# Optimization experiments

Measured on AMD Instinct MI355X. Metric: run time of the kernel, lower is better.

The kernel has to match this reference:

```python
import jax, jax.numpy as jnp
import numpy as np

B, N, D, H, L = 2, 2048, 512, 8, 2
HD = D // H


def setup_inputs() -> dict:
    key = jax.random.key(0)
    ks = jax.random.split(key, 8)
    s = 0.02
    return {
        "inputs_embeds": jax.random.normal(ks[0], (B, N, D), jnp.float32),
        "pos_emb": jax.random.normal(ks[1], (N, D), jnp.float32) * s,
        "c_attn_w": jax.random.normal(ks[2], (L, D, 3 * D), jnp.float32) * s,
        "c_attn_b": jnp.zeros((L, 3 * D), jnp.float32),
        "out_w": jax.random.normal(ks[3], (L, D, D), jnp.float32) * s,
        "out_b": jnp.zeros((L, D), jnp.float32),
        "ln1_g": jnp.ones((L, D), jnp.float32),
        "ln1_b": jnp.zeros((L, D), jnp.float32),
        "c_fc_w": jax.random.normal(ks[4], (L, D, 4 * D), jnp.float32) * s,
        "c_fc_b": jnp.zeros((L, 4 * D), jnp.float32),
        "c_proj_w": jax.random.normal(ks[5], (L, 4 * D, D), jnp.float32) * s,
        "c_proj_b": jnp.zeros((L, D), jnp.float32),
        "ln2_g": jnp.ones((L, D), jnp.float32),
        "ln2_b": jnp.zeros((L, D), jnp.float32),
    }


def _layernorm(x, g, b, eps=1e-5):
    mu = jnp.mean(x, axis=-1, keepdims=True)
    var = jnp.mean(jnp.square(x - mu), axis=-1, keepdims=True)
    return (x - mu) * jax.lax.rsqrt(var + eps) * g + b


def _gelu_new(x):
    # NewGELUActivation: tanh approximation
    return 0.5 * x * (1.0 + jnp.tanh(jnp.sqrt(2.0 / jnp.pi) * (x + 0.044715 * x ** 3)))


def _attention(x, w_qkv, b_qkv, w_out, b_out, self_mask):
    qkv = x @ w_qkv + b_qkv                      # [B,N,3D]
    q, k, v = jnp.split(qkv, 3, axis=-1)
    def heads(t):
        return t.reshape(B, N, H, HD).transpose(0, 2, 1, 3)  # [B,H,N,HD]
    q, k, v = heads(q), heads(k), heads(v)
    scores = jnp.einsum('bhqd,bhkd->bhqk', q, k) / jnp.sqrt(jnp.float32(HD))
    neg = jnp.finfo(scores.dtype).min
    scores = jnp.where(self_mask, scores, neg)   # exclude-self mask
    attn = jax.nn.softmax(scores, axis=-1)
    o = jnp.einsum('bhqk,bhkd->bhqd', attn, v)
    o = o.transpose(0, 2, 1, 3).reshape(B, N, D)
    return o @ w_out + b_out


def reference(inputs_embeds, pos_emb, c_attn_w, c_attn_b, out_w, out_b,
              ln1_g, ln1_b, c_fc_w, c_fc_b, c_proj_w, c_proj_b, ln2_g, ln2_b):
    self_mask = ~jnp.eye(N, dtype=bool)[None, None]  # [1,1,N,N]
    h = inputs_embeds + pos_emb[None]
    for l in range(L):
        res = h
        x = _layernorm(h, ln1_g[l], ln1_b[l])
        h = _attention(x, c_attn_w[l], c_attn_b[l], out_w[l], out_b[l], self_mask) + res
        res = h
        x = _layernorm(h, ln2_g[l], ln2_b[l])
        x = _gelu_new(x @ c_fc_w[l] + c_fc_b[l])
        h = (x @ c_proj_w[l] + c_proj_b[l]) + res
    return h
```

## Files before the change

kernel.cpp:

```cpp
#include <hip/hip_runtime.h>
#include <hip/hip_bf16.h>
#include <math.h>

#define BB 2
#define NN 2048
#define DD 512
#define HH 8
#define LL 2
#define TT (BB*NN)

typedef short short8 __attribute__((ext_vector_type(8)));
typedef float floatx4 __attribute__((ext_vector_type(4)));

__device__ __forceinline__ unsigned short f2b(float v) {
    union { float f; unsigned u; } x; x.f = v;
    unsigned r = x.u + 0x7fff + ((x.u >> 16) & 1);
    return (unsigned short)(r >> 16);
}

__device__ __forceinline__ void gld16(const unsigned short* g, unsigned short* lds) {
    __builtin_amdgcn_global_load_lds(
        (const __attribute__((address_space(1))) unsigned int*)g,
        (__attribute__((address_space(3))) unsigned int*)lds,
        16, 0, 0);
}

__global__ __launch_bounds__(256) void k_bias_add(const float* __restrict__ src,
                                                  const float* __restrict__ bias,
                                                  float* __restrict__ dst) {
    int i = blockIdx.x * 256 + threadIdx.x;
    dst[i] = src[i] + bias[i & (DD - 1)];
}

template <int EMB>
__global__ __launch_bounds__(256) void k_ln(const float* __restrict__ hin,
                                            unsigned short* __restrict__ xout,
                                            const float* __restrict__ g,
                                            const float* __restrict__ b,
                                            const float* __restrict__ emb,
                                            const float* __restrict__ pos,
                                            float* __restrict__ hout) {
    __shared__ float red[4];
    __shared__ float bc1, bc2;
    int t = blockIdx.x;
    int tid = threadIdx.x;
    int lane = tid & 63, wv = tid >> 6;
    float v0, v1;
    if (EMB) {
        const float* erow = emb + (size_t)t * DD;
        const float* prow = pos + (size_t)(t & (NN - 1)) * DD;
        v0 = erow[tid] + prow[tid];
        v1 = erow[tid + 256] + prow[tid + 256];
        hout[(size_t)t * DD + tid] = v0;
        hout[(size_t)t * DD + tid + 256] = v1;
    } else {
        const float* row = hin + (size_t)t * DD;
        v0 = row[tid];
        v1 = row[tid + 256];
    }

    float s = v0 + v1;
#pragma unroll
    for (int o = 32; o; o >>= 1) s += __shfl_down(s, o, 64);
    if (lane == 0) red[wv] = s;
    __syncthreads();
    if (tid == 0) bc1 = (red[0] + red[1] + red[2] + red[3]) * (1.0f / DD);
    __syncthreads();
    float mu = bc1;
    float d0 = v0 - mu, d1 = v1 - mu;
    s = d0 * d0 + d1 * d1;
#pragma unroll
    for (int o = 32; o; o >>= 1) s += __shfl_down(s, o, 64);
    if (lane == 0) red[wv] = s;
    __syncthreads();
    if (tid == 0) bc2 = (red[0] + red[1] + red[2] + red[3]) * (1.0f / DD);
    __syncthreads();
    float rstd = rsqrtf(bc2 + 1e-5f);
    xout[(size_t)t * DD + tid]       = f2b(d0 * rstd * g[tid] + b[tid]);
    xout[(size_t)t * DD + tid + 256] = f2b(d1 * rstd * g[tid + 256] + b[tid + 256]);
}

__device__ __forceinline__ float gelu_new(float v) {
    const float c = 0.7978845608028654f;
    float u = c * (v + 0.044715f * v * v * v);
    u = fminf(fmaxf(u, -30.0f), 30.0f);
    float e = __builtin_amdgcn_exp2f(2.885390081777927f * u);
    return v * e * __builtin_amdgcn_rcpf(e + 1.0f);
}

#define PL 3145728
__global__ __launch_bounds__(256) void k_wt_all(const float* __restrict__ c_attn_w,
                                                const float* __restrict__ out_w,
                                                const float* __restrict__ c_fc_w,
                                                const float* __restrict__ c_proj_w,
                                                unsigned short* __restrict__ wbuf) {
    __shared__ unsigned short t[64][72];
    int bx = blockIdx.x;
    int l = bx / 768;
    int r = bx - l * 768;
    const float* W; unsigned short* WT; int K, N;
    if (r < 192)      { W = c_attn_w + (size_t)l * 512 * 1536; WT = wbuf + (size_t)l * PL;           K = 512;  N = 1536; }
    else if (r < 256) { r -= 192; W = out_w  + (size_t)l * 512 * 512;  WT = wbuf + (size_t)l * PL + 786432;  K = 512;  N = 512; }
    else if (r < 512) { r -= 256; W = c_fc_w + (size_t)l * 512 * 2048; WT = wbuf + (size_t)l * PL + 1048576; K = 512;  N = 2048; }
    else              { r -= 512; W = c_proj_w + (size_t)l * 2048 * 512; WT = wbuf + (size_t)l * PL + 2097152; K = 2048; N = 512; }
    int tiles_n = N >> 6;
    int n0 = (r % tiles_n) * 64, k0 = (r / tiles_n) * 64;

    int tid = threadIdx.x;
    int rr = tid >> 2;
    int c0 = (tid & 3) * 16;
    const float* src = W + (size_t)(k0 + rr) * N + n0 + c0;
#pragma unroll
    for (int u = 0; u < 4; u++) {
        float4 v = *(const float4*)&src[u * 4];
        t[c0 + u * 4 + 0][rr] = f2b(v.x);
        t[c0 + u * 4 + 1][rr] = f2b(v.y);
        t[c0 + u * 4 + 2][rr] = f2b(v.z);
        t[c0 + u * 4 + 3][rr] = f2b(v.w);
    }
    __syncthreads();
    unsigned short* dst = WT + (size_t)(n0 + rr) * K + k0 + c0;
#pragma unroll
    for (int u = 0; u < 4; u++)
        *(uint2*)&dst[u * 4] = *(const uint2*)&t[rr][c0 + u * 4];
}

template <int ACT, int BF16OUT, int ATOMIC>
__global__ __launch_bounds__(512) void k_mgemm(const unsigned short* __restrict__ Ab,
                                               const unsigned short* __restrict__ Bt,
                                               const float* __restrict__ bias,
                                               float* __restrict__ Cp,
                                               unsigned short* __restrict__ Cb,
                                               int Kfull, int Kchunk, int N) {
    __shared__ unsigned short Als[2][16 * 512];
    __shared__ unsigned short Bls[2][16 * 512];

    int tid = threadIdx.x;
    int l = tid & 63, w = tid >> 6;
    int wm = w >> 2, wn = w & 3;
    int m0 = blockIdx.y * 128, n0 = blockIdx.x * 128;
    int kb = blockIdx.z * Kchunk;
    int lr = l & 15;
    int lk = (l >> 4) * 8;

    const unsigned short* Ap = Ab + (size_t)(m0 + w * 16 + lr) * Kfull + kb + lk;
    const unsigned short* Bp = Bt + (size_t)(n0 + w * 16 + lr) * Kfull + kb + lk;
    unsigned short* lsA = &Als[0][0];
    unsigned short* lsB = &Bls[0][0];
    int wbase = w << 9;
    const int KH = 8 * 512;
    const int BUF = 16 * 512;

    floatx4 acc[4][2];
#pragma unroll
    for (int i = 0; i < 4; i++)
#pragma unroll
        for (int j = 0; j < 2; j++) acc[i][j] = (floatx4){0.f, 0.f, 0.f, 0.f};

    int nit = Kchunk >> 6;

    gld16(Ap,      lsA + wbase);
    gld16(Ap + 32, lsA + KH + wbase);
    gld16(Bp,      lsB + wbase);
    gld16(Bp + 32, lsB + KH + wbase);
    __syncthreads();

    for (int it = 0; it < nit; it++) {
        int c = it & 1;
        if (it + 1 < nit) {
            int ko = (it + 1) << 6;
            int db = (c ^ 1) * BUF;
            gld16(Ap + ko,      lsA + db + wbase);
            gld16(Ap + ko + 32, lsA + db + KH + wbase);
            gld16(Bp + ko,      lsB + db + wbase);
            gld16(Bp + ko + 32, lsB + db + KH + wbase);
        }
        int cb = c * BUF;
#pragma unroll
        for (int kk = 0; kk < 2; kk++) {
            short8 a[4], b[2];
            int ko = cb + kk * KH;
#pragma unroll
            for (int i = 0; i < 4; i++)
                a[i] = *(const short8*)&lsA[ko + (wm * 4 + i) * 512 + l * 8];
#pragma unroll
            for (int j = 0; j < 2; j++)
                b[j] = *(const short8*)&lsB[ko + (wn * 2 + j) * 512 + l * 8];
#pragma unroll
            for (int i = 0; i < 4; i++)
#pragma unroll
                for (int j = 0; j < 2; j++)
                    acc[i][j] = __builtin_amdgcn_mfma_f32_16x16x32_bf16(a[i], b[j], acc[i][j], 0, 0, 0);
        }
        __syncthreads();
    }

    int col_in = l & 15, rquad = (l >> 4) * 4;
    bool addb = (!ATOMIC) || (bias != nullptr && blockIdx.z == 0);
#pragma unroll
    for (int i = 0; i < 4; i++) {
        int gm_base = m0 + wm * 64 + i * 16 + rquad;
#pragma unroll
        for (int j = 0; j < 2; j++) {
            int gn = n0 + wn * 32 + j * 16 + col_in;
            float bv = addb ? bias[gn] : 0.0f;
#pragma unroll
            for (int r = 0; r < 4; r++) {
                size_t off = (size_t)(gm_base + r) * N + gn;
                if (ATOMIC) {
                    atomicAdd(&Cp[off], acc[i][j][r] + bv);
                } else {
                    float v = acc[i][j][r] + bv;
                    if (ACT) v = gelu_new(v);
                    if (BF16OUT) Cb[off] = f2b(v);
                    else Cp[off] = v;
                }
            }
        }
    }
}

__global__ __launch_bounds__(256) void k_attn_mfma(const unsigned short* __restrict__ qkv,
                                                   unsigned short* __restrict__ xatt) {
    __shared__ unsigned short Ks[2][64 * 72];
    __shared__ unsigned short Vt[2][64 * 72];
    __shared__ unsigned short Pls[64 * 72];

    int qt = blockIdx.x, hd = blockIdx.y, b = blockIdx.z;
    int tid = threadIdx.x;
    int l = tid & 63, w = tid >> 6;
    int lr = l & 15, quad = l >> 4;

    const size_t base = (size_t)b * NN * 1536;

    short8 qf[2];
    {
        const unsigned short* qrow = qkv + base + (size_t)(qt * 64 + w * 16 + lr) * 1536 + hd * 64;
        qf[0] = *(const short8*)&qrow[quad * 8];
        qf[1] = *(const short8*)&qrow[quad * 8 + 32];
    }

    floatx4 O[4];
#pragma unroll
    for (int jd = 0; jd < 4; jd++) O[jd] = (floatx4){0.f, 0.f, 0.f, 0.f};
    float lsum = 0.0f;

    int sr = tid >> 2, sc = (tid & 3) * 16;
    int vk = (tid & 15) * 4, vd = (tid >> 4) * 4;
    const int STEP = 64 * 1536;
    const unsigned short* Kp = qkv + base + 512 + hd * 64 + (size_t)sr * 1536 + sc;
    const unsigned short* Vp = qkv + base + 1024 + hd * 64 + (size_t)vk * 1536 + vd;

    uint4 rk0, rk1;
    union { uint2 u; unsigned short s[4]; } rv[4];

    rk0 = *(const uint4*)Kp;
    rk1 = *(const uint4*)(Kp + 8);
#pragma unroll
    for (int i = 0; i < 4; i++)
        rv[i].u = *(const uint2*)(Vp + (size_t)i * 1536);
    *(uint4*)&Ks[0][sr * 72 + sc]     = rk0;
    *(uint4*)&Ks[0][sr * 72 + sc + 8] = rk1;
#pragma unroll
    for (int j = 0; j < 4; j++) {
        union { uint2 u; unsigned short s[4]; } pk;
        pk.s[0] = rv[0].s[j]; pk.s[1] = rv[1].s[j];
        pk.s[2] = rv[2].s[j]; pk.s[3] = rv[3].s[j];
        *(uint2*)&Vt[0][(vd + j) * 72 + vk] = pk.u;
    }
    Kp += STEP; Vp += STEP;
    rk0 = *(const uint4*)Kp;
    rk1 = *(const uint4*)(Kp + 8);
#pragma unroll
    for (int i = 0; i < 4; i++)
        rv[i].u = *(const uint2*)(Vp + (size_t)i * 1536);
    __syncthreads();

    const float EC1 = 0.18033688011112042f;
    const float EC0 = -11.541560327111707f;

    for (int kt = 0; kt < 32; kt++) {
        int c = kt & 1;

        floatx4 s[4];
#pragma unroll
        for (int jn = 0; jn < 4; jn++) s[jn] = (floatx4){0.f, 0.f, 0.f, 0.f};
#pragma unroll
        for (int ss = 0; ss < 2; ss++)
#pragma unroll
            for (int jn = 0; jn < 4; jn++) {
                short8 ak = *(const short8*)&Ks[c][(jn * 16 + lr) * 72 + ss * 32 + quad * 8];
                s[jn] = __builtin_amdgcn_mfma_f32_16x16x32_bf16(ak, qf[ss], s[jn], 0, 0, 0);
            }

        int mq = w * 16 + lr;
        bool diag = (kt == qt);
#pragma unroll
        for (int jn = 0; jn < 4; jn++) {
            float p0 = __builtin_amdgcn_exp2f(fmaf(s[jn][0], EC1, EC0));
            float p1 = __builtin_amdgcn_exp2f(fmaf(s[jn][1], EC1, EC0));
            float p2 = __builtin_amdgcn_exp2f(fmaf(s[jn][2], EC1, EC0));
            float p3 = __builtin_amdgcn_exp2f(fmaf(s[jn][3], EC1, EC0));
            if (diag) {
                int kbase = jn * 16 + quad * 4;
                if (mq == kbase + 0) p0 = 0.0f;
                if (mq == kbase + 1) p1 = 0.0f;
                if (mq == kbase + 2) p2 = 0.0f;
                if (mq == kbase + 3) p3 = 0.0f;
            }
            lsum += (p0 + p1) + (p2 + p3);
            unsigned w01, w23;
            asm("v_cvt_pk_bf16_f32 %0, %1, %2" : "=v"(w01) : "v"(p0), "v"(p1));
            asm("v_cvt_pk_bf16_f32 %0, %1, %2" : "=v"(w23) : "v"(p2), "v"(p3));
            uint2 pku; pku.x = w01; pku.y = w23;
            *(uint2*)&Pls[mq * 72 + jn * 16 + quad * 4] = pku;
        }

#pragma unroll
        for (int ss = 0; ss < 2; ss++) {
            short8 ap = *(const short8*)&Pls[(w * 16 + lr) * 72 + ss * 32 + quad * 8];
#pragma unroll
            for (int jd = 0; jd < 4; jd++) {
                short8 bv = *(const short8*)&Vt[c][(jd * 16 + lr) * 72 + ss * 32 + quad * 8];
                O[jd] = __builtin_amdgcn_mfma_f32_16x16x32_bf16(ap, bv, O[jd], 0, 0, 0);
            }
        }

        if (kt < 31) {
            *(uint4*)&Ks[c ^ 1][sr * 72 + sc]     = rk0;
            *(uint4*)&Ks[c ^ 1][sr * 72 + sc + 8] = rk1;
#pragma unroll
            for (int j = 0; j < 4; j++) {
                union { uint2 u; unsigned short s[4]; } pk;
                pk.s[0] = rv[0].s[j]; pk.s[1] = rv[1].s[j];
                pk.s[2] = rv[2].s[j]; pk.s[3] = rv[3].s[j];
                *(uint2*)&Vt[c ^ 1][(vd + j) * 72 + vk] = pk.u;
            }
            if (kt < 30) {
                Kp += STEP; Vp += STEP;
                rk0 = *(const uint4*)Kp;
                rk1 = *(const uint4*)(Kp + 8);
#pragma unroll
                for (int i = 0; i < 4; i++)
                    rv[i].u = *(const uint2*)(Vp + (size_t)i * 1536);
            }
        }
        __syncthreads();
    }

    lsum += __shfl_xor(lsum, 16);
    lsum += __shfl_xor(lsum, 32);
#pragma unroll
    for (int r = 0; r < 4; r++) {
        float inv = 1.0f / __shfl(lsum, quad * 4 + r, 16);
        size_t tok = (size_t)b * NN + qt * 64 + w * 16 + quad * 4 + r;
#pragma unroll
        for (int jd = 0; jd < 4; jd++)
            xatt[tok * DD + hd * 64 + jd * 16 + lr] = f2b(O[jd][r] * inv);
    }
}

extern "C" void kernel_launch(void* const* d_in, const int* in_sizes, int n_in,
                              void* d_out, int out_size, void* d_ws, size_t ws_size,
                              hipStream_t stream) {
    const float* emb      = (const float*)d_in[0];
    const float* pos      = (const float*)d_in[1];
    const float* c_attn_w = (const float*)d_in[2];
    const float* c_attn_b = (const float*)d_in[3];
    const float* out_w    = (const float*)d_in[4];
    const float* out_b    = (const float*)d_in[5];
    const float* ln1_g    = (const float*)d_in[6];
    const float* ln1_b    = (const float*)d_in[7];
    const float* c_fc_w   = (const float*)d_in[8];
    const float* c_fc_b   = (const float*)d_in[9];
    const float* c_proj_w = (const float*)d_in[10];
    const float* c_proj_b = (const float*)d_in[11];
    const float* ln2_g    = (const float*)d_in[12];
    const float* ln2_b    = (const float*)d_in[13];

    char* p = (char*)d_ws;
    float* h = (float*)p;                       p += (size_t)TT * DD * 4;
    unsigned short* act = (unsigned short*)p;   p += (size_t)TT * 2048 * 2;
    unsigned short* x = (unsigned short*)p;     p += (size_t)TT * DD * 2;
    unsigned short* xatt = (unsigned short*)p;  p += (size_t)TT * DD * 2;
    unsigned short* wbuf = (unsigned short*)p;

    unsigned short* qkvb = act;
    unsigned short* ffa  = act;
    float* out = (float*)d_out;

    k_wt_all<<<1536, 256, 0, stream>>>(c_attn_w, out_w, c_fc_w, c_proj_w, wbuf);

    for (int l = 0; l < LL; l++) {
        unsigned short* wqkv_t  = wbuf + (size_t)l * PL;
        unsigned short* wout_t  = wqkv_t + 786432;
        unsigned short* wfc_t   = wqkv_t + 1048576;
        unsigned short* wproj_t = wqkv_t + 2097152;

        if (l == 0)
            k_ln<1><<<TT, 256, 0, stream>>>(nullptr, x, ln1_g, ln1_b, emb, pos, h);
        else
            k_ln<0><<<TT, 256, 0, stream>>>(h, x, ln1_g + l * DD, ln1_b + l * DD,
                                            nullptr, nullptr, nullptr);
        k_mgemm<0, 1, 0><<<dim3(1536 / 128, TT / 128), 512, 0, stream>>>(
            x, wqkv_t, c_attn_b + l * 1536, nullptr, qkvb, 512, 512, 1536);
        k_attn_mfma<<<dim3(NN / 64, HH, BB), 256, 0, stream>>>(qkvb, xatt);
        k_mgemm<0, 0, 1><<<dim3(512 / 128, TT / 128, 2), 512, 0, stream>>>(
            xatt, wout_t, out_b + l * DD, h, nullptr, 512, 256, 512);
        k_ln<0><<<TT, 256, 0, stream>>>(h, x, ln2_g + l * DD, ln2_b + l * DD,
                                        nullptr, nullptr, nullptr);
        k_mgemm<1, 1, 0><<<dim3(2048 / 128, TT / 128), 512, 0, stream>>>(
            x, wfc_t, c_fc_b + l * 2048, nullptr, ffa, 512, 512, 2048);
        if (l == LL - 1) {
            k_bias_add<<<TT * DD / 256, 256, 0, stream>>>(h, c_proj_b + l * DD, out);
            k_mgemm<0, 0, 1><<<dim3(512 / 128, TT / 128, 4), 512, 0, stream>>>(
                ffa, wproj_t, nullptr, out, nullptr, 2048, 512, 512);
        } else {
            k_mgemm<0, 0, 1><<<dim3(512 / 128, TT / 128, 4), 512, 0, stream>>>(
                ffa, wproj_t, c_proj_b + l * DD, h, nullptr, 2048, 512, 512);
        }
    }
}
```

Before: 410.5 us.

## Split attention key tiles across two wave groups with 512-thread blocks

The attention kernel now launches 512 threads per block. Each group of four waves handles half of every 64-key tile: it computes half of the score columns and does half of the PV reduction. One group loads K and the other loads V, and the partial outputs and row sums are combined through shared memory at the end. The goal is more waves per block to hide latency and spread the softmax and MFMA work. The cost is extra LDS traffic, a final reduction step, and more register pressure per block.

```diff
diff --git a/kernel.cpp b/kernel.cpp
--- a/kernel.cpp
+++ b/kernel.cpp
@@ -220,7 +220,7 @@
     }
 }
 
-__global__ __launch_bounds__(256) void k_attn_mfma(const unsigned short* __restrict__ qkv,
+__global__ __launch_bounds__(512) void k_attn_mfma(const unsigned short* __restrict__ qkv,
                                                    unsigned short* __restrict__ xatt) {
     __shared__ unsigned short Ks[2][64 * 72];
     __shared__ unsigned short Vt[2][64 * 72];
@@ -229,13 +229,14 @@
     int qt = blockIdx.x, hd = blockIdx.y, b = blockIdx.z;
     int tid = threadIdx.x;
     int l = tid & 63, w = tid >> 6;
+    int wq = w & 3, ks = w >> 2;
     int lr = l & 15, quad = l >> 4;
 
     const size_t base = (size_t)b * NN * 1536;
 
     short8 qf[2];
     {
-        const unsigned short* qrow = qkv + base + (size_t)(qt * 64 + w * 16 + lr) * 1536 + hd * 64;
+        const unsigned short* qrow = qkv + base + (size_t)(qt * 64 + wq * 16 + lr) * 1536 + hd * 64;
         qf[0] = *(const short8*)&qrow[quad * 8];
         qf[1] = *(const short8*)&qrow[quad * 8 + 32];
     }
@@ -245,8 +246,9 @@
     for (int jd = 0; jd < 4; jd++) O[jd] = (floatx4){0.f, 0.f, 0.f, 0.f};
     float lsum = 0.0f;
 
-    int sr = tid >> 2, sc = (tid & 3) * 16;
-    int vk = (tid & 15) * 4, vd = (tid >> 4) * 4;
+    int tid2 = tid & 255;
+    int sr = tid2 >> 2, sc = (tid2 & 3) * 16;
+    int vk = (tid2 & 15) * 4, vd = (tid2 >> 4) * 4;
     const int STEP = 64 * 1536;
     const unsigned short* Kp = qkv + base + 512 + hd * 64 + (size_t)sr * 1536 + sc;
     const unsigned short* Vp = qkv + base + 1024 + hd * 64 + (size_t)vk * 1536 + vd;
@@ -254,55 +256,60 @@
     uint4 rk0, rk1;
     union { uint2 u; unsigned short s[4]; } rv[4];
 
-    rk0 = *(const uint4*)Kp;
-    rk1 = *(const uint4*)(Kp + 8);
-#pragma unroll
-    for (int i = 0; i < 4; i++)
-        rv[i].u = *(const uint2*)(Vp + (size_t)i * 1536);
-    *(uint4*)&Ks[0][sr * 72 + sc]     = rk0;
-    *(uint4*)&Ks[0][sr * 72 + sc + 8] = rk1;
-#pragma unroll
-    for (int j = 0; j < 4; j++) {
-        union { uint2 u; unsigned short s[4]; } pk;
-        pk.s[0] = rv[0].s[j]; pk.s[1] = rv[1].s[j];
-        pk.s[2] = rv[2].s[j]; pk.s[3] = rv[3].s[j];
-        *(uint2*)&Vt[0][(vd + j) * 72 + vk] = pk.u;
-    }
-    Kp += STEP; Vp += STEP;
-    rk0 = *(const uint4*)Kp;
-    rk1 = *(const uint4*)(Kp + 8);
-#pragma unroll
-    for (int i = 0; i < 4; i++)
-        rv[i].u = *(const uint2*)(Vp + (size_t)i * 1536);
+    if (ks == 0) {
+        rk0 = *(const uint4*)Kp;
+        rk1 = *(const uint4*)(Kp + 8);
+        *(uint4*)&Ks[0][sr * 72 + sc]     = rk0;
+        *(uint4*)&Ks[0][sr * 72 + sc + 8] = rk1;
+        Kp += STEP;
+        rk0 = *(const uint4*)Kp;
+        rk1 = *(const uint4*)(Kp + 8);
+    } else {
+#pragma unroll
+        for (int i = 0; i < 4; i++)
+            rv[i].u = *(const uint2*)(Vp + (size_t)i * 1536);
+#pragma unroll
+        for (int j = 0; j < 4; j++) {
+            union { uint2 u; unsigned short s[4]; } pk;
+            pk.s[0] = rv[0].s[j]; pk.s[1] = rv[1].s[j];
+            pk.s[2] = rv[2].s[j]; pk.s[3] = rv[3].s[j];
+            *(uint2*)&Vt[0][(vd + j) * 72 + vk] = pk.u;
+        }
+        Vp += STEP;
+#pragma unroll
+        for (int i = 0; i < 4; i++)
+            rv[i].u = *(const uint2*)(Vp + (size_t)i * 1536);
+    }
     __syncthreads();
 
     const float EC1 = 0.18033688011112042f;
     const float EC0 = -11.541560327111707f;
 
+    int mq = wq * 16 + lr;
+
     for (int kt = 0; kt < 32; kt++) {
         int c = kt & 1;
 
-        floatx4 s[4];
-#pragma unroll
-        for (int jn = 0; jn < 4; jn++) s[jn] = (floatx4){0.f, 0.f, 0.f, 0.f};
+        floatx4 s[2];
+        s[0] = (floatx4){0.f, 0.f, 0.f, 0.f};
+        s[1] = (floatx4){0.f, 0.f, 0.f, 0.f};
 #pragma unroll
         for (int ss = 0; ss < 2; ss++)
 #pragma unroll
-            for (int jn = 0; jn < 4; jn++) {
-                short8 ak = *(const short8*)&Ks[c][(jn * 16 + lr) * 72 + ss * 32 + quad * 8];
-                s[jn] = __builtin_amdgcn_mfma_f32_16x16x32_bf16(ak, qf[ss], s[jn], 0, 0, 0);
+            for (int jnn = 0; jnn < 2; jnn++) {
+                short8 ak = *(const short8*)&Ks[c][((ks * 2 + jnn) * 16 + lr) * 72 + ss * 32 + quad * 8];
+                s[jnn] = __builtin_amdgcn_mfma_f32_16x16x32_bf16(ak, qf[ss], s[jnn], 0, 0, 0);
             }
 
-        int mq = w * 16 + lr;
         bool diag = (kt == qt);
 #pragma unroll
-        for (int jn = 0; jn < 4; jn++) {
-            float p0 = __builtin_amdgcn_exp2f(fmaf(s[jn][0], EC1, EC0));
-            float p1 = __builtin_amdgcn_exp2f(fmaf(s[jn][1], EC1, EC0));
-            float p2 = __builtin_amdgcn_exp2f(fmaf(s[jn][2], EC1, EC0));
-            float p3 = __builtin_amdgcn_exp2f(fmaf(s[jn][3], EC1, EC0));
+        for (int jnn = 0; jnn < 2; jnn++) {
+            float p0 = __builtin_amdgcn_exp2f(fmaf(s[jnn][0], EC1, EC0));
+            float p1 = __builtin_amdgcn_exp2f(fmaf(s[jnn][1], EC1, EC0));
+            float p2 = __builtin_amdgcn_exp2f(fmaf(s[jnn][2], EC1, EC0));
+            float p3 = __builtin_amdgcn_exp2f(fmaf(s[jnn][3], EC1, EC0));
             if (diag) {
-                int kbase = jn * 16 + quad * 4;
+                int kbase = (ks * 2 + jnn) * 16 + quad * 4;
                 if (mq == kbase + 0) p0 = 0.0f;
                 if (mq == kbase + 1) p1 = 0.0f;
                 if (mq == kbase + 2) p2 = 0.0f;
@@ -313,50 +320,72 @@
             asm("v_cvt_pk_bf16_f32 %0, %1, %2" : "=v"(w01) : "v"(p0), "v"(p1));
             asm("v_cvt_pk_bf16_f32 %0, %1, %2" : "=v"(w23) : "v"(p2), "v"(p3));
             uint2 pku; pku.x = w01; pku.y = w23;
-            *(uint2*)&Pls[mq * 72 + jn * 16 + quad * 4] = pku;
-        }
-
-#pragma unroll
-        for (int ss = 0; ss < 2; ss++) {
-            short8 ap = *(const short8*)&Pls[(w * 16 + lr) * 72 + ss * 32 + quad * 8];
+            *(uint2*)&Pls[mq * 72 + (ks * 2 + jnn) * 16 + quad * 4] = pku;
+        }
+
+        {
+            short8 ap = *(const short8*)&Pls[(wq * 16 + lr) * 72 + ks * 32 + quad * 8];
 #pragma unroll
             for (int jd = 0; jd < 4; jd++) {
-                short8 bv = *(const short8*)&Vt[c][(jd * 16 + lr) * 72 + ss * 32 + quad * 8];
+                short8 bv = *(const short8*)&Vt[c][(jd * 16 + lr) * 72 + ks * 32 + quad * 8];
                 O[jd] = __builtin_amdgcn_mfma_f32_16x16x32_bf16(ap, bv, O[jd], 0, 0, 0);
             }
         }
 
         if (kt < 31) {
-            *(uint4*)&Ks[c ^ 1][sr * 72 + sc]     = rk0;
-            *(uint4*)&Ks[c ^ 1][sr * 72 + sc + 8] = rk1;
-#pragma unroll
-            for (int j = 0; j < 4; j++) {
-                union { uint2 u; unsigned short s[4]; } pk;
-                pk.s[0] = rv[0].s[j]; pk.s[1] = rv[1].s[j];
-                pk.s[2] = rv[2].s[j]; pk.s[3] = rv[3].s[j];
-                *(uint2*)&Vt[c ^ 1][(vd + j) * 72 + vk] = pk.u;
+            if (ks == 0) {
+                *(uint4*)&Ks[c ^ 1][sr * 72 + sc]     = rk0;
+                *(uint4*)&Ks[c ^ 1][sr * 72 + sc + 8] = rk1;
+                if (kt < 30) {
+                    Kp += STEP;
+                    rk0 = *(const uint4*)Kp;
+                    rk1 = *(const uint4*)(Kp + 8);
+                }
+            } else {
+#pragma unroll
+                for (int j = 0; j < 4; j++) {
+                    union { uint2 u; unsigned short s[4]; } pk;
+                    pk.s[0] = rv[0].s[j]; pk.s[1] = rv[1].s[j];
+                    pk.s[2] = rv[2].s[j]; pk.s[3] = rv[3].s[j];
+                    *(uint2*)&Vt[c ^ 1][(vd + j) * 72 + vk] = pk.u;
+                }
+                if (kt < 30) {
+                    Vp += STEP;
+#pragma unroll
+                    for (int i = 0; i < 4; i++)
+                        rv[i].u = *(const uint2*)(Vp + (size_t)i * 1536);
+                }
             }
-            if (kt < 30) {
-                Kp += STEP; Vp += STEP;
-                rk0 = *(const uint4*)Kp;
-                rk1 = *(const uint4*)(Kp + 8);
-#pragma unroll
-                for (int i = 0; i < 4; i++)
-                    rv[i].u = *(const uint2*)(Vp + (size_t)i * 1536);
-            }
         }
         __syncthreads();
     }
+
+    float* Obuf = (float*)&Ks[0][0];
+    float* lsumbuf = (float*)&Vt[0][0];
 
     lsum += __shfl_xor(lsum, 16);
     lsum += __shfl_xor(lsum, 32);
-#pragma unroll
-    for (int r = 0; r < 4; r++) {
-        float inv = 1.0f / __shfl(lsum, quad * 4 + r, 16);
-        size_t tok = (size_t)b * NN + qt * 64 + w * 16 + quad * 4 + r;
-#pragma unroll
-        for (int jd = 0; jd < 4; jd++)
-            xatt[tok * DD + hd * 64 + jd * 16 + lr] = f2b(O[jd][r] * inv);
+
+    if (ks == 1) {
+        if (quad == 0) lsumbuf[wq * 16 + lr] = lsum;
+#pragma unroll
+        for (int r = 0; r < 4; r++)
+#pragma unroll
+            for (int jd = 0; jd < 4; jd++)
+                Obuf[(wq * 16 + quad * 4 + r) * 64 + jd * 16 + lr] = O[jd][r];
+    }
+    __syncthreads();
+    if (ks == 0) {
+        lsum += lsumbuf[wq * 16 + lr];
+#pragma unroll
+        for (int r = 0; r < 4; r++) {
+            float inv = 1.0f / __shfl(lsum, quad * 4 + r, 16);
+            size_t tok = (size_t)b * NN + qt * 64 + wq * 16 + quad * 4 + r;
+#pragma unroll
+            for (int jd = 0; jd < 4; jd++)
+                xatt[tok * DD + hd * 64 + jd * 16 + lr] =
+                    f2b((O[jd][r] + Obuf[(wq * 16 + quad * 4 + r) * 64 + jd * 16 + lr]) * inv);
+        }
     }
 }
 
@@ -404,7 +433,7 @@
                                             nullptr, nullptr, nullptr);
         k_mgemm<0, 1, 0><<<dim3(1536 / 128, TT / 128), 512, 0, stream>>>(
             x, wqkv_t, c_attn_b + l * 1536, nullptr, qkvb, 512, 512, 1536);
-        k_attn_mfma<<<dim3(NN / 64, HH, BB), 256, 0, stream>>>(qkvb, xatt);
+        k_attn_mfma<<<dim3(NN / 64, HH, BB), 512, 0, stream>>>(qkvb, xatt);
         k_mgemm<0, 0, 1><<<dim3(512 / 128, TT / 128, 2), 512, 0, stream>>>(
             xatt, wout_t, out_b + l * DD, h, nullptr, 512, 256, 512);
         k_ln<0><<<TT, 256, 0, stream>>>(h, x, ln2_g + l * DD, ln2_b + l * DD,
```

New measurement: 414.3 us. About the same (+0.9%).
